# Kernel tuning notes

Measured on AMD Instinct MI355X. Metric: run time of the kernel, lower is better.

## Reference

```python
import jax, jax.numpy as jnp
import numpy as np

B, S, C = 4, 4096, 1024
H, D, K = 16, 64, 256  # nhead, head_dim, dim_k


def setup_inputs() -> dict:
    key = jax.random.key(0)
    ks = jax.random.split(key, 7)
    x = jax.random.normal(ks[0], (B, S, C), dtype=jnp.float32)
    # per-head QKV projection weights (torch Linear weight layout [out,in])
    Wq = jax.random.normal(ks[1], (H, D, C), dtype=jnp.float32) * (C ** -0.5)
    Wk = jax.random.normal(ks[2], (H, D, C), dtype=jnp.float32) * (C ** -0.5)
    Wv = jax.random.normal(ks[3], (H, D, C), dtype=jnp.float32) * (C ** -0.5)
    # Linformer E/F sequence projections, per head: [K, S]
    We = jax.random.normal(ks[4], (H, K, S), dtype=jnp.float32) * (S ** -0.5)
    Wf = jax.random.normal(ks[5], (H, K, S), dtype=jnp.float32) * (S ** -0.5)
    # output projection (with bias, as w_o is nn.Linear default bias=True)
    Wo = jax.random.normal(ks[6], (C, H * D), dtype=jnp.float32) * ((H * D) ** -0.5)
    bo = jnp.zeros((C,), dtype=jnp.float32)
    return {"x": x, "Wq": Wq, "Wk": Wk, "Wv": Wv, "We": We, "Wf": Wf, "Wo": Wo, "bo": bo}


def reference(x, Wq, Wk, Wv, We, Wf, Wo, bo):
    # per-head projections: [B,H,S,D]
    Q = jnp.einsum('bsc,hdc->bhsd', x, Wq)
    Kh = jnp.einsum('bsc,hdc->bhsd', x, Wk)
    Vh = jnp.einsum('bsc,hdc->bhsd', x, Wv)
    # E-projection of K over the sequence axis: K^T [B,H,D,S] -> [B,H,D,K]
    Kp = jnp.einsum('bhsd,hks->bhdk', Kh, We)
    # scores: Q @ E(K^T) / sqrt(head_dim), softmax over low-rank axis k
    scale = 1.0 / jnp.sqrt(jnp.asarray(D, dtype=x.dtype))
    P = jax.nn.softmax(jnp.einsum('bhsd,bhdk->bhsk', Q, Kp) * scale, axis=-1)
    # F-projection of V over the sequence axis, then transpose back: [B,H,K,D]
    Vp = jnp.einsum('bhsd,hks->bhkd', Vh, Wf)
    out = jnp.einsum('bhsk,bhkd->bhsd', P, Vp)          # [B,H,S,D]
    out = out.transpose(0, 2, 1, 3).reshape(B, S, H * D)  # concat heads
    return jnp.einsum('bse,ce->bsc', out, Wo) + bo       # w_o (dropout=0)
```

## Files before the change

kernel.cpp:

```cpp
#include <hip/hip_runtime.h>
#include <stdint.h>


typedef unsigned short u16;
typedef __bf16 bf16t;
typedef bf16t bf16x8 __attribute__((ext_vector_type(8)));
typedef float f32x4 __attribute__((ext_vector_type(4)));
typedef u16 u16x8 __attribute__((ext_vector_type(8)));

#define MFMA16(a, b, c) __builtin_amdgcn_mfma_f32_16x16x32_bf16((a), (b), (c), 0, 0, 0)

__device__ __forceinline__ u16 f2bf(float f) {
  return __builtin_bit_cast(u16, (bf16t)f);
}

__device__ __forceinline__ bf16x8 ldf(const u16* p) { return *(const bf16x8*)p; }

__device__ __forceinline__ void gload16(const void* g, void* l) {
  __builtin_amdgcn_global_load_lds(
      (__attribute__((address_space(1))) void*)g,
      (__attribute__((address_space(3))) void*)l, 16, 0, 0);
}

__device__ __forceinline__ int xcd_swz(int orig, int nwg) {
  return (orig & 7) * (nwg >> 3) + (orig >> 3);
}

__device__ __forceinline__ void gemm256_main(const u16* __restrict__ A,
                                             const u16* __restrict__ BT,
                                             int m0, int n0, f32x4 acc[8][4],
                                             u16* sm) {
  const int tid = threadIdx.x;
  const int w = tid >> 6, l = tid & 63, g = l >> 4, r = l & 15;
  const int wr = w >> 2, wc = w & 3;
  const int rowt = tid >> 3;
  const int cbsw = ((tid & 7) * 16) ^ ((rowt & 7) << 4);
  const int sxor = (r & 7) << 4;
  const char* Ab = (const char*)A;
  const char* Bb = (const char*)BT;
  char* smc = (char*)sm;

  auto stage = [&](int T, int buf) {
    const int k0 = T * 64;
#pragma unroll
    for (int i = 0; i < 4; ++i) {
      const int row = i * 64 + rowt;
      gload16(Ab + (((size_t)(m0 + row) << 10) + k0) * 2 + cbsw,
              smc + buf * 32768 + i * 8192 + w * 1024);
      gload16(Bb + (((size_t)(n0 + row) << 10) + k0) * 2 + cbsw,
              smc + 65536 + buf * 32768 + i * 8192 + w * 1024);
    }
  };

  stage(0, 0);
  for (int t = 0; t < 16; ++t) {
    const int b = t & 1;
    stage(t < 15 ? t + 1 : 15, b ^ 1);
    asm volatile("s_waitcnt vmcnt(8)" ::: "memory");
    __builtin_amdgcn_s_barrier();
    asm volatile("" ::: "memory");
    const char* At = smc + b * 32768;
    const char* Bt = smc + 65536 + b * 32768;
#pragma unroll
    for (int kk = 0; kk < 2; ++kk) {
      const int cb = (kk * 64 + g * 16) ^ sxor;
      bf16x8 af[8], bf[4];
#pragma unroll
      for (int m = 0; m < 8; ++m)
        af[m] = *(const bf16x8*)(At + ((wr * 128 + m * 16 + r) * 128 + cb));
#pragma unroll
      for (int n = 0; n < 4; ++n)
        bf[n] = *(const bf16x8*)(Bt + ((wc * 64 + n * 16 + r) * 128 + cb));
      __builtin_amdgcn_s_setprio(1);
#pragma unroll
      for (int m = 0; m < 8; ++m)
#pragma unroll
        for (int n = 0; n < 4; ++n)
          acc[m][n] = MFMA16(af[m], bf[n], acc[m][n]);
      __builtin_amdgcn_s_setprio(0);
    }
    asm volatile("" ::: "memory");
    __builtin_amdgcn_s_barrier();
    asm volatile("" ::: "memory");
  }
}

__global__ __launch_bounds__(256) void cvt_x(const float* __restrict__ src,
                                             u16* __restrict__ dst) {
  const size_t i = ((size_t)blockIdx.x * 256 + threadIdx.x) * 8;
  const float4 a = *(const float4*)(src + i);
  const float4 b = *(const float4*)(src + i + 4);
  u16x8 o;
  o[0] = f2bf(a.x); o[1] = f2bf(a.y); o[2] = f2bf(a.z); o[3] = f2bf(a.w);
  o[4] = f2bf(b.x); o[5] = f2bf(b.y); o[6] = f2bf(b.z); o[7] = f2bf(b.w);
  *(u16x8*)(dst + i) = o;
}

__global__ __launch_bounds__(256) void cvt_w(const float* __restrict__ Wq,
                                             const float* __restrict__ Wk,
                                             const float* __restrict__ Wv,
                                             const float* __restrict__ Wo,
                                             u16* __restrict__ wqkv,
                                             u16* __restrict__ wob) {
  const float* s;
  u16* d;
  switch (blockIdx.y) {
    case 0: s = Wq; d = wqkv; break;
    case 1: s = Wk; d = wqkv + 1048576; break;
    case 2: s = Wv; d = wqkv + 2097152; break;
    default: s = Wo; d = wob; break;
  }
  const size_t i = ((size_t)blockIdx.x * 256 + threadIdx.x) * 8;
  const float4 a = *(const float4*)(s + i);
  const float4 b = *(const float4*)(s + i + 4);
  u16x8 o;
  o[0] = f2bf(a.x); o[1] = f2bf(a.y); o[2] = f2bf(a.z); o[3] = f2bf(a.w);
  o[4] = f2bf(b.x); o[5] = f2bf(b.y); o[6] = f2bf(b.z); o[7] = f2bf(b.w);
  *(u16x8*)(d + i) = o;
}

__global__ __launch_bounds__(512, 2) void gemm_q(const u16* __restrict__ A,
                                                 const u16* __restrict__ BT,
                                                 u16* __restrict__ Qd) {
  __shared__ u16 sm[65536];
  const int wg = xcd_swz(blockIdx.x, 256);
  const int m0 = (wg >> 2) * 256, n0 = (wg & 3) * 256;
  const int tid = threadIdx.x, w = tid >> 6, l = tid & 63, g = l >> 4, r = l & 15;
  const int wr = w >> 2, wc = w & 3;
  f32x4 acc[8][4] = {};
  gemm256_main(A, BT, m0, n0, acc, sm);
#pragma unroll
  for (int m = 0; m < 8; ++m)
#pragma unroll
    for (int n = 0; n < 4; ++n)
#pragma unroll
      for (int j = 0; j < 4; ++j) {
        const int mm = m0 + wr * 128 + m * 16 + g * 4 + j;
        const int nn = n0 + wc * 64 + n * 16 + r;
        const int b = mm >> 12, s = mm & 4095, h = nn >> 6, d = nn & 63;
        Qd[(((size_t)(b * 16 + h)) * 4096 + s) * 64 + d] = f2bf(acc[m][n][j] * 0.125f);
      }
}

__global__ __launch_bounds__(512, 2) void gemm_kv(const u16* __restrict__ A,
                                                  const u16* __restrict__ BT,
                                                  u16* __restrict__ KTd,
                                                  u16* __restrict__ VTd) {
  __shared__ u16 sm[65536];
  const int wg = xcd_swz(blockIdx.x, 512);
  const int m0 = (wg & 7) * 256, n0 = (wg >> 3) * 256;
  const int tid = threadIdx.x, w = tid >> 6, l = tid & 63, g = l >> 4, r = l & 15;
  const int wr = w >> 2, wc = w & 3;
  f32x4 acc[8][4] = {};
  gemm256_main(A, BT, m0, n0, acc, sm);
#pragma unroll
  for (int m = 0; m < 8; ++m)
#pragma unroll
    for (int n = 0; n < 4; ++n)
#pragma unroll
      for (int j = 0; j < 4; ++j) {
        const int mm = m0 + wr * 128 + m * 16 + g * 4 + j;
        const int nn = n0 + wc * 64 + n * 16 + r;
        const int which = mm >> 10, hd = mm & 1023, h = hd >> 6, d = hd & 63;
        const int b = nn >> 12, s = nn & 4095;
        u16* dst = which ? VTd : KTd;
        dst[(((size_t)(b * 16 + h)) * 64 + d) * 4096 + s] = f2bf(acc[m][n][j]);
      }
}

__global__ __launch_bounds__(512, 2) void gemm_out(const u16* __restrict__ A,
                                                   const u16* __restrict__ BT,
                                                   const float* __restrict__ bo,
                                                   float* __restrict__ out) {
  __shared__ u16 sm[65536];
  const int wg = xcd_swz(blockIdx.x, 256);
  const int m0 = (wg >> 2) * 256, n0 = (wg & 3) * 256;
  const int tid = threadIdx.x, w = tid >> 6, l = tid & 63, g = l >> 4, r = l & 15;
  const int wr = w >> 2, wc = w & 3;
  f32x4 acc[8][4] = {};
  gemm256_main(A, BT, m0, n0, acc, sm);
#pragma unroll
  for (int m = 0; m < 8; ++m)
#pragma unroll
    for (int n = 0; n < 4; ++n)
#pragma unroll
      for (int j = 0; j < 4; ++j) {
        const int mm = m0 + wr * 128 + m * 16 + g * 4 + j;
        const int nn = n0 + wc * 64 + n * 16 + r;
        out[(size_t)mm * 1024 + nn] = acc[m][n][j] + bo[nn];
      }
}

__global__ __launch_bounds__(256) void gemm_small(const float* __restrict__ WeF,
                                                  const float* __restrict__ WfF,
                                                  const u16* __restrict__ KT,
                                                  const u16* __restrict__ VT,
                                                  float* __restrict__ part) {
  __shared__ float ldsW[256 * 64];
  __shared__ u16 ldsS[64 * 64];
  const int bx = blockIdx.x, chunk = blockIdx.y;
  const int mode = bx & 1;
  const int bh = bx >> 1;
  const int hh = bh & 15;
  const float* Wp = (mode == 0 ? WeF : WfF) + (size_t)hh * 256 * 4096;
  const u16* Sp = (mode == 0 ? KT : VT) + (size_t)bh * 64 * 4096;
  float* Cpf = part + ((size_t)(mode * 4 + chunk) * 64 + bh) * 16384;
  const int tid = threadIdx.x, w = tid >> 6, l = tid & 63, g = l >> 4, r = l & 15;
  char* ldsWb = (char*)ldsW;
  char* ldsSb = (char*)ldsS;
  const int wcs = (tid & 15) ^ ((tid >> 4) & 7);
  const int scs = (tid & 7) ^ ((tid >> 3) & 7);
  f32x4 acc[4][4] = {};
  for (int kt = chunk * 16; kt < chunk * 16 + 16; ++kt) {
    const int k0 = kt * 64;
    __syncthreads();
#pragma unroll
    for (int i = 0; i < 16; ++i)
      gload16(Wp + (size_t)(i * 16 + (tid >> 4)) * 4096 + k0 + wcs * 4,
              ldsWb + i * 4096 + w * 1024);
#pragma unroll
    for (int j = 0; j < 2; ++j)
      gload16(Sp + (size_t)(j * 32 + (tid >> 3)) * 4096 + k0 + scs * 8,
              ldsSb + j * 4096 + w * 1024);
    __syncthreads();
    const int m8 = r & 7;
#pragma unroll
    for (int kk = 0; kk < 2; ++kk) {
      bf16x8 wf8[4], sf8[4];
#pragma unroll
      for (int f = 0; f < 4; ++f) {
        const int wrow = w * 64 + f * 16 + r;
        const int c0 = (kk * 8 + g * 2) ^ m8;
        const int c1 = (kk * 8 + g * 2 + 1) ^ m8;
        const f32x4 lo = *(const f32x4*)(ldsWb + wrow * 256 + c0 * 16);
        const f32x4 hi = *(const f32x4*)(ldsWb + wrow * 256 + c1 * 16);
        bf16x8 o;
#pragma unroll
        for (int q = 0; q < 4; ++q) {
          o[q] = (bf16t)lo[q];
          o[q + 4] = (bf16t)hi[q];
        }
        wf8[f] = o;
        const int srow = f * 16 + r;
        const int sc = (kk * 4 + g) ^ m8;
        sf8[f] = *(const bf16x8*)(ldsSb + srow * 128 + sc * 16);
      }
      if (mode == 0) {
#pragma unroll
        for (int fm = 0; fm < 4; ++fm)
#pragma unroll
          for (int fn = 0; fn < 4; ++fn)
            acc[fm][fn] = MFMA16(wf8[fm], sf8[fn], acc[fm][fn]);
      } else {
#pragma unroll
        for (int fm = 0; fm < 4; ++fm)
#pragma unroll
          for (int fn = 0; fn < 4; ++fn)
            acc[fm][fn] = MFMA16(sf8[fm], wf8[fn], acc[fm][fn]);
      }
    }
  }
  if (mode == 0) {
#pragma unroll
    for (int fm = 0; fm < 4; ++fm)
#pragma unroll
      for (int fn = 0; fn < 4; ++fn)
#pragma unroll
        for (int j = 0; j < 4; ++j)
          Cpf[(size_t)(w * 64 + fm * 16 + g * 4 + j) * 64 + fn * 16 + r] =
              acc[fm][fn][j];
  } else {
#pragma unroll
    for (int fm = 0; fm < 4; ++fm)
#pragma unroll
      for (int fn = 0; fn < 4; ++fn)
#pragma unroll
        for (int j = 0; j < 4; ++j)
          Cpf[(size_t)(fm * 16 + g * 4 + j) * 256 + w * 64 + fn * 16 + r] =
              acc[fm][fn][j];
  }
}

__global__ __launch_bounds__(256) void reduce_small(const float* __restrict__ part,
                                                    u16* __restrict__ Kp,
                                                    u16* __restrict__ VpT) {
  const int i4 = blockIdx.x * 256 + threadIdx.x;
  const int mode = i4 >> 18;
  const int r4 = i4 & 262143;
  const float4* b = (const float4*)part;
  float4 s0 = b[(size_t)(mode * 4 + 0) * 262144 + r4];
  float4 s1 = b[(size_t)(mode * 4 + 1) * 262144 + r4];
  float4 s2 = b[(size_t)(mode * 4 + 2) * 262144 + r4];
  float4 s3 = b[(size_t)(mode * 4 + 3) * 262144 + r4];
  ushort4 o;
  o.x = f2bf(s0.x + s1.x + s2.x + s3.x);
  o.y = f2bf(s0.y + s1.y + s2.y + s3.y);
  o.z = f2bf(s0.z + s1.z + s2.z + s3.z);
  o.w = f2bf(s0.w + s1.w + s2.w + s3.w);
  ushort4* dst = (ushort4*)(mode ? VpT : Kp);
  dst[r4] = o;
}

__global__ __launch_bounds__(256, 1) void attn_fused(const u16* __restrict__ Q,
                                                     const u16* __restrict__ Kp,
                                                     const u16* __restrict__ VpT,
                                                     u16* __restrict__ att) {
  __shared__ u16 P[4][16 * 264];
  const int gid = blockIdx.x;
  const int bh = gid >> 3;
  const int st = gid & 7;
  const int hh = bh & 15, b = bh >> 4;
  const int tid = threadIdx.x, w = tid >> 6, l = tid & 63, g = l >> 4, r = l & 15;
  const u16* Kpb = Kp + (size_t)bh * 256 * 64;
  const u16* Vb = VpT + (size_t)bh * 64 * 256;

  bf16x8 kf[32];
  bf16x8 vf[32];
#pragma unroll
  for (int fn = 0; fn < 16; ++fn) {
    kf[fn * 2 + 0] = ldf(Kpb + (fn * 16 + r) * 64 + g * 8);
    kf[fn * 2 + 1] = ldf(Kpb + (fn * 16 + r) * 64 + 32 + g * 8);
  }
#pragma unroll
  for (int fn2 = 0; fn2 < 4; ++fn2)
#pragma unroll
    for (int kk = 0; kk < 8; ++kk)
      vf[fn2 * 8 + kk] = ldf(Vb + (fn2 * 16 + r) * 256 + kk * 32 + g * 8);

  u16* Pw = P[w];
  for (int t = 0; t < 8; ++t) {
    const int s0 = st * 512 + t * 64 + w * 16;
    const u16* Qb = Q + ((size_t)bh * 4096 + s0) * 64;
    const bf16x8 qf0 = ldf(Qb + r * 64 + g * 8);
    const bf16x8 qf1 = ldf(Qb + r * 64 + 32 + g * 8);
    f32x4 sc[16];
#pragma unroll
    for (int fn = 0; fn < 16; ++fn) {
      sc[fn] = MFMA16(qf0, kf[fn * 2 + 0], (f32x4){});
      sc[fn] = MFMA16(qf1, kf[fn * 2 + 1], sc[fn]);
    }
    float rinv[4];
#pragma unroll
    for (int j = 0; j < 4; ++j) {
      float sum = 0.f;
#pragma unroll
      for (int fn = 0; fn < 16; ++fn) {
        const float e = __expf(sc[fn][j]);
        sc[fn][j] = e;
        sum += e;
      }
      sum += __shfl_xor(sum, 1);
      sum += __shfl_xor(sum, 2);
      sum += __shfl_xor(sum, 4);
      sum += __shfl_xor(sum, 8);
      rinv[j] = 1.0f / sum;
    }
#pragma unroll
    for (int fn = 0; fn < 16; ++fn)
#pragma unroll
      for (int j = 0; j < 4; ++j)
        Pw[(g * 4 + j) * 264 + fn * 16 + r] = f2bf(sc[fn][j]);

    f32x4 o[4] = {};
#pragma unroll
    for (int kk = 0; kk < 8; ++kk) {
      const bf16x8 pa = ldf(Pw + r * 264 + kk * 32 + g * 8);
#pragma unroll
      for (int fn2 = 0; fn2 < 4; ++fn2)
        o[fn2] = MFMA16(pa, vf[fn2 * 8 + kk], o[fn2]);
    }
#pragma unroll
    for (int fn2 = 0; fn2 < 4; ++fn2)
#pragma unroll
      for (int j = 0; j < 4; ++j) {
        const int s = s0 + g * 4 + j;
        const int d = fn2 * 16 + r;
        att[((size_t)b * 4096 + s) * 1024 + hh * 64 + d] = f2bf(o[fn2][j] * rinv[j]);
      }
  }
}

extern "C" void kernel_launch(void* const* d_in, const int* in_sizes, int n_in,
                              void* d_out, int out_size, void* d_ws, size_t ws_size,
                              hipStream_t stream) {
  (void)in_sizes; (void)n_in; (void)out_size; (void)ws_size;
  const float* x  = (const float*)d_in[0];
  const float* Wq = (const float*)d_in[1];
  const float* Wk = (const float*)d_in[2];
  const float* Wv = (const float*)d_in[3];
  const float* We = (const float*)d_in[4];
  const float* Wf = (const float*)d_in[5];
  const float* Wo = (const float*)d_in[6];
  const float* bo = (const float*)d_in[7];
  char* ws = (char*)d_ws;
  u16* xb    = (u16*)(ws + 0);
  float* prt = (float*)(ws + 0);
  u16* att   = (u16*)(ws + 0);
  u16* wqkv  = (u16*)(ws + 33554432);
  u16* wob   = (u16*)(ws + 106954752);
  u16* Qd    = (u16*)(ws + 109051904);
  u16* KTd   = (u16*)(ws + 142606336);
  u16* VTd   = (u16*)(ws + 176160768);
  u16* Kpd   = (u16*)(ws + 209715200);
  u16* VpTd  = (u16*)(ws + 211812352);

  cvt_x<<<8192, 256, 0, stream>>>(x, xb);
  cvt_w<<<dim3(512, 4), 256, 0, stream>>>(Wq, Wk, Wv, Wo, wqkv, wob);
  gemm_q<<<256, 512, 0, stream>>>(xb, wqkv, Qd);
  gemm_kv<<<512, 512, 0, stream>>>(wqkv + 1048576, xb, KTd, VTd);
  gemm_small<<<dim3(128, 4), 256, 0, stream>>>(We, Wf, KTd, VTd, prt);
  reduce_small<<<2048, 256, 0, stream>>>(prt, Kpd, VpTd);
  attn_fused<<<512, 256, 0, stream>>>(Qd, Kpd, VpTd, att);
  gemm_out<<<256, 512, 0, stream>>>(att, wob, bo, (float*)d_out);
}
```

Before: 315.8 us.

## Pipeline GEMM core in half-K chunks and batch Linformer projections across batch

New measurement: 322.9 us. 1.02x slower.

```diff
diff --git a/kernel.cpp b/kernel.cpp
--- a/kernel.cpp
+++ b/kernel.cpp
@@ -26,62 +26,86 @@
   return (orig & 7) * (nwg >> 3) + (orig >> 3);
 }
 
-__device__ __forceinline__ void gemm256_main(const u16* __restrict__ A,
-                                             const u16* __restrict__ BT,
-                                             int m0, int n0, f32x4 acc[8][4],
-                                             u16* sm) {
+__device__ __forceinline__ void gemm256_pipe(const u16* __restrict__ A,
+                                             const u16* __restrict__ B,
+                                             int m0, int n0, int sA1, int sB1,
+                                             int s0, int kt0, f32x4 acc[8][4],
+                                             char* smc) {
   const int tid = threadIdx.x;
   const int w = tid >> 6, l = tid & 63, g = l >> 4, r = l & 15;
   const int wr = w >> 2, wc = w & 3;
-  const int rowt = tid >> 3;
-  const int cbsw = ((tid & 7) * 16) ^ ((rowt & 7) << 4);
-  const int sxor = (r & 7) << 4;
-  const char* Ab = (const char*)A;
-  const char* Bb = (const char*)BT;
-  char* smc = (char*)sm;
-
-  auto stage = [&](int T, int buf) {
-    const int k0 = T * 64;
-#pragma unroll
-    for (int i = 0; i < 4; ++i) {
-      const int row = i * 64 + rowt;
-      gload16(Ab + (((size_t)(m0 + row) << 10) + k0) * 2 + cbsw,
-              smc + buf * 32768 + i * 8192 + w * 1024);
-      gload16(Bb + (((size_t)(n0 + row) << 10) + k0) * 2 + cbsw,
-              smc + 65536 + buf * 32768 + i * 8192 + w * 1024);
+  const int lrow = l >> 2;
+  const int ksw = (((l & 3) ^ (lrow & 3)) << 4);
+  const int gx = ((g ^ (r & 3)) << 4);
+
+  auto stage = [&](const u16* Base, int r0, int s1, int T, int ch, int ldsoff) {
+#pragma unroll
+    for (int i = 0; i < 2; ++i) {
+      const int row = r0 + (w * 2 + i) * 16 + lrow;
+      const size_t eoff = (size_t)(row >> 6) * s1 + (size_t)(row & 63) * s0;
+      gload16((const char*)Base + eoff * 2 + ((kt0 + T) * 64 + ch * 32) * 2 + ksw,
+              smc + ldsoff + (w * 2 + i) * 1024);
     }
   };
 
-  stage(0, 0);
+  stage(A, m0, sA1, 0, 0, 0);
+  stage(B, n0, sB1, 0, 0, 32768);
+  stage(A, m0, sA1, 0, 1, 16384);
+  stage(B, n0, sB1, 0, 1, 32768 + 16384);
+
   for (int t = 0; t < 16; ++t) {
-    const int b = t & 1;
-    stage(t < 15 ? t + 1 : 15, b ^ 1);
-    asm volatile("s_waitcnt vmcnt(8)" ::: "memory");
+    const int buf = (t & 1) << 16, nb = buf ^ 65536;
+    const int Tn = t < 15 ? t + 1 : 15;
+    bf16x8 af[4], bfv[4];
+
+#define QUAD(MH)                                                        \
+  __builtin_amdgcn_s_setprio(1);                                        \
+  _Pragma("unroll") for (int m = 0; m < 4; ++m)                         \
+      _Pragma("unroll") for (int n = 0; n < 4; ++n)                     \
+          acc[(MH)*4 + m][n] = MFMA16(af[m], bfv[n], acc[(MH)*4 + m][n]); \
+  __builtin_amdgcn_s_setprio(0);
+
+    stage(A, m0, sA1, Tn, 0, nb);
+    asm volatile("s_waitcnt vmcnt(6)" ::: "memory");
     __builtin_amdgcn_s_barrier();
     asm volatile("" ::: "memory");
-    const char* At = smc + b * 32768;
-    const char* Bt = smc + 65536 + b * 32768;
-#pragma unroll
-    for (int kk = 0; kk < 2; ++kk) {
-      const int cb = (kk * 64 + g * 16) ^ sxor;
-      bf16x8 af[8], bf[4];
-#pragma unroll
-      for (int m = 0; m < 8; ++m)
-        af[m] = *(const bf16x8*)(At + ((wr * 128 + m * 16 + r) * 128 + cb));
+    {
+      const char* At = smc + buf;
+      const char* Bt = smc + buf + 32768;
 #pragma unroll
       for (int n = 0; n < 4; ++n)
-        bf[n] = *(const bf16x8*)(Bt + ((wc * 64 + n * 16 + r) * 128 + cb));
-      __builtin_amdgcn_s_setprio(1);
-#pragma unroll
-      for (int m = 0; m < 8; ++m)
-#pragma unroll
-        for (int n = 0; n < 4; ++n)
-          acc[m][n] = MFMA16(af[m], bf[n], acc[m][n]);
-      __builtin_amdgcn_s_setprio(0);
-    }
-    asm volatile("" ::: "memory");
+        bfv[n] = *(const bf16x8*)(Bt + (wc * 64 + n * 16 + r) * 64 + gx);
+#pragma unroll
+      for (int m = 0; m < 4; ++m)
+        af[m] = *(const bf16x8*)(At + (wr * 128 + m * 16 + r) * 64 + gx);
+      QUAD(0)
+      stage(B, n0, sB1, Tn, 0, nb + 32768);
+#pragma unroll
+      for (int m = 0; m < 4; ++m)
+        af[m] = *(const bf16x8*)(At + (wr * 128 + 64 + m * 16 + r) * 64 + gx);
+      QUAD(1)
+    }
+    stage(A, m0, sA1, Tn, 1, nb + 16384);
+    asm volatile("s_waitcnt vmcnt(6)" ::: "memory");
     __builtin_amdgcn_s_barrier();
     asm volatile("" ::: "memory");
+    {
+      const char* At = smc + buf + 16384;
+      const char* Bt = smc + buf + 32768 + 16384;
+#pragma unroll
+      for (int n = 0; n < 4; ++n)
+        bfv[n] = *(const bf16x8*)(Bt + (wc * 64 + n * 16 + r) * 64 + gx);
+#pragma unroll
+      for (int m = 0; m < 4; ++m)
+        af[m] = *(const bf16x8*)(At + (wr * 128 + m * 16 + r) * 64 + gx);
+      QUAD(0)
+      stage(B, n0, sB1, Tn, 1, nb + 32768 + 16384);
+#pragma unroll
+      for (int m = 0; m < 4; ++m)
+        af[m] = *(const bf16x8*)(At + (wr * 128 + 64 + m * 16 + r) * 64 + gx);
+      QUAD(1)
+    }
+#undef QUAD
   }
 }
 
@@ -119,6 +143,21 @@
   *(u16x8*)(d + i) = o;
 }
 
+__global__ __launch_bounds__(256) void cvt_wef(const float* __restrict__ We,
+                                               const float* __restrict__ Wf,
+                                               u16* __restrict__ web,
+                                               u16* __restrict__ wfb) {
+  const float* s = blockIdx.y ? Wf : We;
+  u16* d = blockIdx.y ? wfb : web;
+  const size_t i = ((size_t)blockIdx.x * 256 + threadIdx.x) * 8;
+  const float4 a = *(const float4*)(s + i);
+  const float4 b = *(const float4*)(s + i + 4);
+  u16x8 o;
+  o[0] = f2bf(a.x); o[1] = f2bf(a.y); o[2] = f2bf(a.z); o[3] = f2bf(a.w);
+  o[4] = f2bf(b.x); o[5] = f2bf(b.y); o[6] = f2bf(b.z); o[7] = f2bf(b.w);
+  *(u16x8*)(d + i) = o;
+}
+
 __global__ __launch_bounds__(512, 2) void gemm_q(const u16* __restrict__ A,
                                                  const u16* __restrict__ BT,
                                                  u16* __restrict__ Qd) {
@@ -128,7 +167,7 @@
   const int tid = threadIdx.x, w = tid >> 6, l = tid & 63, g = l >> 4, r = l & 15;
   const int wr = w >> 2, wc = w & 3;
   f32x4 acc[8][4] = {};
-  gemm256_main(A, BT, m0, n0, acc, sm);
+  gemm256_pipe(A, BT, m0, n0, 65536, 65536, 1024, 0, acc, (char*)sm);
 #pragma unroll
   for (int m = 0; m < 8; ++m)
 #pragma unroll
@@ -152,7 +191,7 @@
   const int tid = threadIdx.x, w = tid >> 6, l = tid & 63, g = l >> 4, r = l & 15;
   const int wr = w >> 2, wc = w & 3;
   f32x4 acc[8][4] = {};
-  gemm256_main(A, BT, m0, n0, acc, sm);
+  gemm256_pipe(A, BT, m0, n0, 65536, 65536, 1024, 0, acc, (char*)sm);
 #pragma unroll
   for (int m = 0; m < 8; ++m)
 #pragma unroll
@@ -178,7 +217,7 @@
   const int tid = threadIdx.x, w = tid >> 6, l = tid & 63, g = l >> 4, r = l & 15;
   const int wr = w >> 2, wc = w & 3;
   f32x4 acc[8][4] = {};
-  gemm256_main(A, BT, m0, n0, acc, sm);
+  gemm256_pipe(A, BT, m0, n0, 65536, 65536, 1024, 0, acc, (char*)sm);
 #pragma unroll
   for (int m = 0; m < 8; ++m)
 #pragma unroll
@@ -191,114 +230,64 @@
       }
 }
 
-__global__ __launch_bounds__(256) void gemm_small(const float* __restrict__ WeF,
-                                                  const float* __restrict__ WfF,
-                                                  const u16* __restrict__ KT,
-                                                  const u16* __restrict__ VT,
-                                                  float* __restrict__ part) {
-  __shared__ float ldsW[256 * 64];
-  __shared__ u16 ldsS[64 * 64];
-  const int bx = blockIdx.x, chunk = blockIdx.y;
-  const int mode = bx & 1;
-  const int bh = bx >> 1;
-  const int hh = bh & 15;
-  const float* Wp = (mode == 0 ? WeF : WfF) + (size_t)hh * 256 * 4096;
-  const u16* Sp = (mode == 0 ? KT : VT) + (size_t)bh * 64 * 4096;
-  float* Cpf = part + ((size_t)(mode * 4 + chunk) * 64 + bh) * 16384;
+__global__ __launch_bounds__(512, 2) void gemm_small(const u16* __restrict__ web,
+                                                     const u16* __restrict__ wfb,
+                                                     const u16* __restrict__ KT,
+                                                     const u16* __restrict__ VT,
+                                                     float* __restrict__ part) {
+  __shared__ u16 sm[65536];
+  const int bx = blockIdx.x;
+  const int h = bx & 15, mode = (bx >> 4) & 1, chunk = bx >> 5;
+  const u16 *Ab, *Bb;
+  int sA1, sB1;
+  if (mode == 0) {
+    Ab = web + (size_t)h * 1048576; sA1 = 262144;
+    Bb = KT + (size_t)h * 262144;   sB1 = 4194304;
+  } else {
+    Ab = VT + (size_t)h * 262144;   sA1 = 4194304;
+    Bb = wfb + (size_t)h * 1048576; sB1 = 262144;
+  }
+  f32x4 acc[8][4] = {};
+  gemm256_pipe(Ab, Bb, 0, 0, sA1, sB1, 4096, chunk * 16, acc, (char*)sm);
+  float* Cp = part + ((size_t)((mode * 4 + chunk) * 16 + h)) * 65536;
   const int tid = threadIdx.x, w = tid >> 6, l = tid & 63, g = l >> 4, r = l & 15;
-  char* ldsWb = (char*)ldsW;
-  char* ldsSb = (char*)ldsS;
-  const int wcs = (tid & 15) ^ ((tid >> 4) & 7);
-  const int scs = (tid & 7) ^ ((tid >> 3) & 7);
-  f32x4 acc[4][4] = {};
-  for (int kt = chunk * 16; kt < chunk * 16 + 16; ++kt) {
-    const int k0 = kt * 64;
-    __syncthreads();
-#pragma unroll
-    for (int i = 0; i < 16; ++i)
-      gload16(Wp + (size_t)(i * 16 + (tid >> 4)) * 4096 + k0 + wcs * 4,
-              ldsWb + i * 4096 + w * 1024);
-#pragma unroll
-    for (int j = 0; j < 2; ++j)
-      gload16(Sp + (size_t)(j * 32 + (tid >> 3)) * 4096 + k0 + scs * 8,
-              ldsSb + j * 4096 + w * 1024);
-    __syncthreads();
-    const int m8 = r & 7;
-#pragma unroll
-    for (int kk = 0; kk < 2; ++kk) {
-      bf16x8 wf8[4], sf8[4];
-#pragma unroll
-      for (int f = 0; f < 4; ++f) {
-        const int wrow = w * 64 + f * 16 + r;
-        const int c0 = (kk * 8 + g * 2) ^ m8;
-        const int c1 = (kk * 8 + g * 2 + 1) ^ m8;
-        const f32x4 lo = *(const f32x4*)(ldsWb + wrow * 256 + c0 * 16);
-        const f32x4 hi = *(const f32x4*)(ldsWb + wrow * 256 + c1 * 16);
-        bf16x8 o;
-#pragma unroll
-        for (int q = 0; q < 4; ++q) {
-          o[q] = (bf16t)lo[q];
-          o[q + 4] = (bf16t)hi[q];
-        }
-        wf8[f] = o;
-        const int srow = f * 16 + r;
-        const int sc = (kk * 4 + g) ^ m8;
-        sf8[f] = *(const bf16x8*)(ldsSb + srow * 128 + sc * 16);
-      }
-      if (mode == 0) {
-#pragma unroll
-        for (int fm = 0; fm < 4; ++fm)
-#pragma unroll
-          for (int fn = 0; fn < 4; ++fn)
-            acc[fm][fn] = MFMA16(wf8[fm], sf8[fn], acc[fm][fn]);
-      } else {
-#pragma unroll
-        for (int fm = 0; fm < 4; ++fm)
-#pragma unroll
-          for (int fn = 0; fn < 4; ++fn)
-            acc[fm][fn] = MFMA16(sf8[fm], wf8[fn], acc[fm][fn]);
-      }
-    }
-  }
-  if (mode == 0) {
-#pragma unroll
-    for (int fm = 0; fm < 4; ++fm)
-#pragma unroll
-      for (int fn = 0; fn < 4; ++fn)
-#pragma unroll
-        for (int j = 0; j < 4; ++j)
-          Cpf[(size_t)(w * 64 + fm * 16 + g * 4 + j) * 64 + fn * 16 + r] =
-              acc[fm][fn][j];
-  } else {
-#pragma unroll
-    for (int fm = 0; fm < 4; ++fm)
-#pragma unroll
-      for (int fn = 0; fn < 4; ++fn)
-#pragma unroll
-        for (int j = 0; j < 4; ++j)
-          Cpf[(size_t)(fm * 16 + g * 4 + j) * 256 + w * 64 + fn * 16 + r] =
-              acc[fm][fn][j];
-  }
+  const int wr = w >> 2, wc = w & 3;
+#pragma unroll
+  for (int m = 0; m < 8; ++m)
+#pragma unroll
+    for (int n = 0; n < 4; ++n)
+#pragma unroll
+      for (int j = 0; j < 4; ++j)
+        Cp[(size_t)(wr * 128 + m * 16 + g * 4 + j) * 256 + wc * 64 + n * 16 + r] =
+            acc[m][n][j];
 }
 
 __global__ __launch_bounds__(256) void reduce_small(const float* __restrict__ part,
                                                     u16* __restrict__ Kp,
                                                     u16* __restrict__ VpT) {
-  const int i4 = blockIdx.x * 256 + threadIdx.x;
-  const int mode = i4 >> 18;
-  const int r4 = i4 & 262143;
-  const float4* b = (const float4*)part;
-  float4 s0 = b[(size_t)(mode * 4 + 0) * 262144 + r4];
-  float4 s1 = b[(size_t)(mode * 4 + 1) * 262144 + r4];
-  float4 s2 = b[(size_t)(mode * 4 + 2) * 262144 + r4];
-  float4 s3 = b[(size_t)(mode * 4 + 3) * 262144 + r4];
+  const int i = blockIdx.x * 256 + threadIdx.x;
+  const int mode = i >> 18;
+  const int rem = i & 262143;
+  const int h = rem >> 14;
+  const int e = (rem & 16383) * 4;
+  const int m = e >> 8, n = e & 255;
+  const float* pb = part + ((size_t)mode * 64 + h) * 65536 + e;
+  const float4 s0 = *(const float4*)(pb);
+  const float4 s1 = *(const float4*)(pb + 1048576);
+  const float4 s2 = *(const float4*)(pb + 2097152);
+  const float4 s3 = *(const float4*)(pb + 3145728);
   ushort4 o;
   o.x = f2bf(s0.x + s1.x + s2.x + s3.x);
   o.y = f2bf(s0.y + s1.y + s2.y + s3.y);
   o.z = f2bf(s0.z + s1.z + s2.z + s3.z);
   o.w = f2bf(s0.w + s1.w + s2.w + s3.w);
-  ushort4* dst = (ushort4*)(mode ? VpT : Kp);
-  dst[r4] = o;
+  if (mode == 0) {
+    const int b = n >> 6, d = n & 63;
+    *(ushort4*)(Kp + ((size_t)(b * 16 + h)) * 16384 + m * 64 + d) = o;
+  } else {
+    const int b = m >> 6, d = m & 63;
+    *(ushort4*)(VpT + ((size_t)(b * 16 + h)) * 16384 + d * 256 + n) = o;
+  }
 }
 
 __global__ __launch_bounds__(256, 1) void attn_fused(const u16* __restrict__ Q,
@@ -397,6 +386,8 @@
   float* prt = (float*)(ws + 0);
   u16* att   = (u16*)(ws + 0);
   u16* wqkv  = (u16*)(ws + 33554432);
+  u16* web   = (u16*)(ws + 39845888);
+  u16* wfb   = (u16*)(ws + 73400320);
   u16* wob   = (u16*)(ws + 106954752);
   u16* Qd    = (u16*)(ws + 109051904);
   u16* KTd   = (u16*)(ws + 142606336);
@@ -406,9 +397,10 @@
 
   cvt_x<<<8192, 256, 0, stream>>>(x, xb);
   cvt_w<<<dim3(512, 4), 256, 0, stream>>>(Wq, Wk, Wv, Wo, wqkv, wob);
+  cvt_wef<<<dim3(8192, 2), 256, 0, stream>>>(We, Wf, web, wfb);
   gemm_q<<<256, 512, 0, stream>>>(xb, wqkv, Qd);
   gemm_kv<<<512, 512, 0, stream>>>(wqkv + 1048576, xb, KTd, VTd);
-  gemm_small<<<dim3(128, 4), 256, 0, stream>>>(We, Wf, KTd, VTd, prt);
+  gemm_small<<<128, 512, 0, stream>>>(web, wfb, KTd, VTd, prt);
   reduce_small<<<2048, 256, 0, stream>>>(prt, Kpd, VpTd);
   attn_fused<<<512, 256, 0, stream>>>(Qd, Kpd, VpTd, att);
   gemm_out<<<256, 512, 0, stream>>>(att, wob, bo, (float*)d_out);
```
